# Optimization experiments

Measured on AMD Instinct MI355X. Metric: run time of the kernel, lower is better.

## Reference

```python
import jax, jax.numpy as jnp
import numpy as np

B = 64        # graphs per batch
N = 2048      # nodes per graph
BN = B * N
BE = BN * 16  # edges (avg degree 16)
C1 = 64
C2 = 64
M = 16
K_EDGES = 4   # hardcoded k=4 in original forward


def setup_inputs() -> dict:
    key = jax.random.key(0)
    k1, k2, k3, k4, k5, k6 = jax.random.split(key, 6)
    x = jax.random.normal(k1, (BN, C1), dtype=jnp.float32)
    e_ = jax.random.randint(k2, (2, BE), 0, BN, dtype=jnp.int32)
    b_ = jnp.repeat(jnp.arange(B, dtype=jnp.int32), N)  # sorted batch index
    # Linear params (stored as (in, out); torch stores (out, in))
    W_assign = jax.random.normal(k3, (C1, M), dtype=jnp.float32) / np.sqrt(C1)
    b_assign = jax.random.normal(k4, (M,), dtype=jnp.float32) * 0.01
    W_embed = jax.random.normal(k5, (C1, C2 - 3), dtype=jnp.float32) / np.sqrt(C1)
    b_embed = jax.random.normal(k6, (C2 - 3,), dtype=jnp.float32) * 0.01
    return {"x": x, "e_": e_, "b_": b_, "W_assign": W_assign,
            "b_assign": b_assign, "W_embed": W_embed, "b_embed": b_embed}


def reference(x, e_, b_, W_assign, b_assign, W_embed, b_embed):
    BN_, _ = x.shape
    Bn = int(jnp.max(b_)) + 1
    Mm = W_assign.shape[1]

    p = x[:, :3]                                   # (BN, 3) positions
    f = x @ W_embed + b_embed                      # (BN, C2-3)
    S = jax.nn.softmax(x @ W_assign + b_assign, axis=-1)  # (BN, M)

    # Weighted scatter-reduce pooling: index_add over (batch*M + m)
    # == per-batch segment_sum of S[n,m] * feat[n,c]
    Zf = jax.ops.segment_sum(S[:, :, None] * f[:, None, :], b_, num_segments=Bn)  # (B, M, C2-3)
    Zp = jax.ops.segment_sum(S[:, :, None] * p[:, None, :], b_, num_segments=Bn)  # (B, M, 3)
    w = jax.ops.segment_sum(S, b_, num_segments=Bn)                               # (B, M)
    w = jnp.maximum(w, 1e-10)
    Zp = Zp / w[..., None]
    x_out = jnp.concatenate([Zp, Zf], axis=-1).reshape(Bn * Mm, -1)  # (B*M, C2)

    # Sparse adjacency pooling: AS = A_NN @ S (A_NN[src,dst]=1 per edge)
    AS = jax.ops.segment_sum(S[e_[1]], e_[0], num_segments=BN_)  # (BN, M)
    # A_MM[b] = (S^T masked to batch b) @ AS
    A_MM = jax.ops.segment_sum(S[:, :, None] * AS[:, None, :], b_, num_segments=Bn)  # (B, M, M)

    # top-k edge construction on pooled adjacency
    dst = jax.lax.top_k(A_MM, K_EDGES)[1]                                # (B, M, k)
    src = jnp.broadcast_to(jnp.arange(Mm)[None, :, None], (Bn, Mm, K_EDGES))
    offset = (jnp.arange(Bn) * Mm)[:, None, None]
    e_out = jnp.stack([(src + offset).reshape(-1), (dst + offset).reshape(-1)], axis=0)
    b_out = jnp.repeat(jnp.arange(Bn), Mm)
    return x_out, e_out, b_out
```

## Files before the change

kernel.cpp:

```cpp
#include <hip/hip_runtime.h>

#define BN 131072
#define BE 2097152
#define NGR 64
#define CAP 36864

#define XS_OFF     0
#define WACC_OFF   262144
#define A_OFF      266240
#define ZERO_U4    20736
#define CUR_OFF    331776
#define QS_OFF     332032
#define ENDS_OFF   333056
#define SH_OFF     2430208
#define PK_OFF     6624512

__device__ __forceinline__ float bflo(unsigned u) { return __uint_as_float(u << 16); }
__device__ __forceinline__ float bfhi(unsigned u) { return __uint_as_float(u & 0xFFFF0000u); }

__global__ __launch_bounds__(256) void k_zero(uint4* __restrict__ zbase,
                                              int* __restrict__ cur)
{
    int zi = blockIdx.x * 256 + threadIdx.x;
    if (zi < ZERO_U4) zbase[zi] = make_uint4(0u, 0u, 0u, 0u);
    if (blockIdx.x == 0 && threadIdx.x < NGR) cur[threadIdx.x] = threadIdx.x * CAP;
}

__global__ __launch_bounds__(256) void k_scatter(const int* __restrict__ e_,
                                                 int* __restrict__ cur,
                                                 unsigned* __restrict__ packed)
{
    __shared__ int h[64];
    __shared__ int gb[64];
    int t = threadIdx.x;
    if (t < 64) h[t] = 0;
    __syncthreads();
    size_t base = (size_t)blockIdx.x * 4096;
    int e0v[16], e1v[16], rk[16];
    #pragma unroll
    for (int k = 0; k < 16; ++k) {
        size_t i = base + k * 256 + t;
        e0v[k] = e_[i];
        e1v[k] = e_[BE + i];
        rk[k] = atomicAdd(&h[e0v[k] >> 11], 1);
    }
    __syncthreads();
    if (t < 64) gb[t] = atomicAdd(&cur[t], h[t]);
    __syncthreads();
    #pragma unroll
    for (int k = 0; k < 16; ++k) {
        int b = e0v[k] >> 11;
        packed[gb[b] + rk[k]] = ((unsigned)(e0v[k] & 2047) << 17) | (unsigned)e1v[k];
    }
}

__global__ __launch_bounds__(256) void k_nodeSort(const float* __restrict__ x,
                                                  const float* __restrict__ Wa,
                                                  const float* __restrict__ ba,
                                                  unsigned short* __restrict__ Sh,
                                                  float* __restrict__ Xs,
                                                  float* __restrict__ wacc,
                                                  unsigned* __restrict__ packed,
                                                  const int* __restrict__ cur,
                                                  int* __restrict__ qs,
                                                  int* __restrict__ ends4)
{
    __shared__ __align__(16) unsigned char smem[47616];
    const int t = threadIdx.x;
    const int blk = blockIdx.x;

    if (blk < 256) {
        unsigned* sout = (unsigned*)smem;
        int* h    = (int*)(smem + 36864);
        int* psum = (int*)(smem + 45056);
        const int Q = blk;
        const int g = Q >> 2;
        const int q = Q & 3;
        const int slab = g * CAP;
        const int n = cur[g] - slab;
        const int chunk = (n + 3) >> 2;
        const int qlo = slab + min(q * chunk, n);
        const int qhi = slab + min((q + 1) * chunk, n);
        const int nq = qhi - qlo;
        if (t == 0) qs[Q] = qlo;

        for (int i = t; i < 2048; i += 256) h[i] = 0;
        __syncthreads();
        for (int i = t; i < nq; i += 256) {
            atomicAdd(&h[packed[qlo + i] >> 17], 1);
        }
        __syncthreads();

        int hl[8]; int s = 0;
        #pragma unroll
        for (int j = 0; j < 8; ++j) { hl[j] = h[t * 8 + j]; s += hl[j]; }
        psum[t] = s;
        __syncthreads();
        for (int off = 1; off < 256; off <<= 1) {
            int v = (t >= off) ? psum[t - off] : 0;
            __syncthreads();
            psum[t] += v;
            __syncthreads();
        }
        int run = psum[t] - s;
        int* ends = ends4 + (Q << 11);
        #pragma unroll
        for (int j = 0; j < 8; ++j) {
            int bin = t * 8 + j;
            int c = hl[j];
            h[bin] = run;
            run += c;
            ends[bin] = qlo + run;
        }
        __syncthreads();
        for (int i = t; i < nq; i += 256) {
            unsigned u = packed[qlo + i];
            int pos = atomicAdd(&h[u >> 17], 1);
            sout[pos] = u & 131071u;
        }
        __syncthreads();
        for (int i = t; i < nq; i += 256) packed[qlo + i] = sout[i];
        return;
    }

    const int nblk = blk - 256;
    const int g = nblk >> 4;
    float* Xl = (float*)smem;
    float* Sl = (float*)(smem + 33280);
    float* Wl = (float*)(smem + 43520);
    const int nd = t & 127;
    const int ch = t >> 7;

    const float4* xg4 = (const float4*)(x + (size_t)nblk * 128 * 64);
    #pragma unroll
    for (int it = 0; it < 8; ++it) {
        int idx4 = it * 256 + t;
        float4 v = xg4[idx4];
        int node = idx4 >> 4;
        int c4 = (idx4 & 15) * 4;
        float* p = &Xl[node * 65 + c4];
        p[0] = v.x; p[1] = v.y; p[2] = v.z; p[3] = v.w;
    }
    for (int i = t; i < 1024; i += 256) Wl[i] = Wa[i];
    __syncthreads();

    float lg[16];
    #pragma unroll
    for (int m = 0; m < 16; ++m) lg[m] = 0.f;
    const int c0 = ch * 32;
    for (int c = c0; c < c0 + 32; ++c) {
        float xc = Xl[nd * 65 + c];
        #pragma unroll
        for (int m = 0; m < 16; ++m) lg[m] += xc * Wl[c * 16 + m];
    }
    float* Pl = Sl;
    if (ch == 1) {
        #pragma unroll
        for (int m = 0; m < 16; ++m) Pl[nd * 17 + m] = lg[m];
    }
    __syncthreads();

    float s[16];
    if (ch == 0) {
        float sum = 0.f, mx;
        #pragma unroll
        for (int m = 0; m < 16; ++m) lg[m] += ba[m] + Pl[nd * 17 + m];
        mx = lg[0];
        #pragma unroll
        for (int m = 1; m < 16; ++m) mx = fmaxf(mx, lg[m]);
        #pragma unroll
        for (int m = 0; m < 16; ++m) { s[m] = __expf(lg[m] - mx); sum += s[m]; }
        float inv = 1.f / sum;
        #pragma unroll
        for (int m = 0; m < 16; ++m) s[m] *= inv;

        unsigned pk8[8];
        #pragma unroll
        for (int j = 0; j < 8; ++j) {
            unsigned b0 = __float_as_uint(s[2*j]);
            unsigned b1 = __float_as_uint(s[2*j+1]);
            unsigned h0 = (b0 + 0x7FFFu + ((b0 >> 16) & 1u)) >> 16;
            unsigned h1 = (b1 + 0x7FFFu + ((b1 >> 16) & 1u)) >> 16;
            pk8[j] = h0 | (h1 << 16);
        }
        uint4* hrow = (uint4*)(Sh + ((size_t)nblk * 128 + nd) * 16);
        hrow[0] = make_uint4(pk8[0], pk8[1], pk8[2], pk8[3]);
        hrow[1] = make_uint4(pk8[4], pk8[5], pk8[6], pk8[7]);
    }
    __syncthreads();
    if (ch == 0) {
        #pragma unroll
        for (int q = 0; q < 4; ++q)
            *(float4*)(&Sl[nd * 20 + q * 4]) = make_float4(s[q*4], s[q*4+1], s[q*4+2], s[q*4+3]);
    }
    __syncthreads();

    const int c = t & 63;
    const int mg = t >> 6;
    float a0 = 0.f, a1 = 0.f, a2 = 0.f, a3 = 0.f;
    for (int n = 0; n < 128; ++n) {
        float xv = Xl[n * 65 + c];
        float4 sa = *(const float4*)(&Sl[n * 20 + mg * 4]);
        a0 += sa.x * xv; a1 += sa.y * xv; a2 += sa.z * xv; a3 += sa.w * xv;
    }
    float* xsg = Xs + g * 1024 + (mg * 4) * 64 + c;
    atomicAdd(&xsg[0],   a0);
    atomicAdd(&xsg[64],  a1);
    atomicAdd(&xsg[128], a2);
    atomicAdd(&xsg[192], a3);

    if (t < 16) {
        float ws_ = 0.f;
        for (int n = 0; n < 128; ++n) ws_ += Sl[n * 20 + t];
        atomicAdd(&wacc[g * 16 + t], ws_);
    }
}

__global__ __launch_bounds__(256) void k_edge(const unsigned* __restrict__ se1,
                                              const unsigned short* __restrict__ Sh,
                                              const int* __restrict__ ends4,
                                              const int* __restrict__ qs,
                                              float* __restrict__ A)
{
    __shared__ __align__(16) float ASl[64 * 16];
    const int t = threadIdx.x;
    const int blk = blockIdx.x;
    const int g = blk >> 5;
    const int nbase = blk << 6;

    {
        const int qd = t >> 2;
        const int c4 = (t & 3) << 2;
        const int nl = (nbase & 2047) + qd;
        const unsigned short* __restrict__ ShB = Sh + c4;

        int lo[4], hi[4];
        #pragma unroll
        for (int q = 0; q < 4; ++q) {
            const int Qb = (g << 2) + q;
            const int* __restrict__ ends = ends4 + (Qb << 11);
            lo[q] = nl ? ends[nl - 1] : qs[Qb];
            hi[q] = ends[nl];
        }

        float a0 = 0.f, a1 = 0.f, a2 = 0.f, a3 = 0.f;
        #pragma unroll
        for (int q = 0; q < 4; ++q) {
            int i = lo[q];
            const int h2 = hi[q];
            for (; i + 4 <= h2; i += 4) {
                unsigned ea = se1[i];
                unsigned eb = se1[i + 1];
                unsigned ec = se1[i + 2];
                unsigned ed = se1[i + 3];
                uint2 ra = *(const uint2*)(ShB + ((size_t)ea << 4));
                uint2 rb = *(const uint2*)(ShB + ((size_t)eb << 4));
                uint2 rc = *(const uint2*)(ShB + ((size_t)ec << 4));
                uint2 rd = *(const uint2*)(ShB + ((size_t)ed << 4));
                a0 += bflo(ra.x) + bflo(rb.x) + bflo(rc.x) + bflo(rd.x);
                a1 += bfhi(ra.x) + bfhi(rb.x) + bfhi(rc.x) + bfhi(rd.x);
                a2 += bflo(ra.y) + bflo(rb.y) + bflo(rc.y) + bflo(rd.y);
                a3 += bfhi(ra.y) + bfhi(rb.y) + bfhi(rc.y) + bfhi(rd.y);
            }
            for (; i < h2; ++i) {
                unsigned ea = se1[i];
                uint2 ra = *(const uint2*)(ShB + ((size_t)ea << 4));
                a0 += bflo(ra.x); a1 += bfhi(ra.x); a2 += bflo(ra.y); a3 += bfhi(ra.y);
            }
        }
        *(float4*)(&ASl[qd * 16 + c4]) = make_float4(a0, a1, a2, a3);
    }
    __syncthreads();

    {
        const int m = t >> 4;
        const int k = t & 15;
        const unsigned short* __restrict__ SgM = Sh + ((size_t)nbase << 4) + m;
        float a = 0.f;
        #pragma unroll 4
        for (int i = 0; i < 64; ++i) {
            float sv = __uint_as_float((unsigned)SgM[(size_t)i << 4] << 16);
            a += sv * ASl[i * 16 + k];
        }
        atomicAdd(&A[(g << 8) + t], a);
    }
}

__global__ __launch_bounds__(256) void k_xt(const float* __restrict__ Xs,
                                            const float* __restrict__ wacc,
                                            const float* __restrict__ We,
                                            const float* __restrict__ be,
                                            const float* __restrict__ A,
                                            float* __restrict__ out)
{
    __shared__ float WeL[64 * 61];
    const int t = threadIdx.x;
    const int blk = blockIdx.x;
    for (int i = t; i < 64 * 61; i += 256) WeL[i] = We[i];
    __syncthreads();

    if (blk < 256) {
        int lane = t & 63;
        int row = blk * 4 + (t >> 6);
        const float* xs = Xs + row * 64;
        float w = wacc[row];
        float val;
        if (lane < 3) {
            val = xs[lane] / fmaxf(w, 1e-10f);
        } else {
            int c2 = lane - 3;
            float accv = w * be[c2];
            for (int cc = 0; cc < 64; ++cc) accv += xs[cc] * WeL[cc * 61 + c2];
            val = accv;
        }
        out[row * 64 + lane] = val;
    } else {
        int r = (blk - 256) * 256 + t;
        float v[16];
        #pragma unroll
        for (int i = 0; i < 16; ++i) v[i] = A[r * 16 + i];
        float* e0o = out + 65536;
        float* e1o = out + 65536 + 4096;
        float* bo  = out + 65536 + 8192;
        unsigned mask = 0;
        #pragma unroll
        for (int rep = 0; rep < 4; ++rep) {
            float best = -3.4e38f; int bi = 0;
            #pragma unroll
            for (int i = 0; i < 16; ++i) {
                bool ok = (((mask >> i) & 1u) == 0u) && (v[i] > best);
                if (ok) { best = v[i]; bi = i; }
            }
            mask |= (1u << bi);
            e0o[r * 4 + rep] = (float)r;
            e1o[r * 4 + rep] = (float)((r & ~15) + bi);
        }
        bo[r] = (float)(r >> 4);
    }
}

extern "C" void kernel_launch(void* const* d_in, const int* in_sizes, int n_in,
                              void* d_out, int out_size, void* d_ws, size_t ws_size,
                              hipStream_t stream)
{
    const float* x  = (const float*)d_in[0];
    const int*   e  = (const int*)d_in[1];
    const float* Wa = (const float*)d_in[3];
    const float* ba = (const float*)d_in[4];
    const float* We = (const float*)d_in[5];
    const float* be = (const float*)d_in[6];

    char* ws = (char*)d_ws;
    float* Xs     = (float*)(ws + XS_OFF);
    float* wacc   = (float*)(ws + WACC_OFF);
    float* A      = (float*)(ws + A_OFF);
    int*   cur    = (int*)(ws + CUR_OFF);
    int*   qs     = (int*)(ws + QS_OFF);
    int*   ends4  = (int*)(ws + ENDS_OFF);
    unsigned short* Sh = (unsigned short*)(ws + SH_OFF);
    unsigned* packed = (unsigned*)(ws + PK_OFF);

    k_zero    <<<82, 256, 0, stream>>>((uint4*)ws, cur);
    k_scatter <<<512, 256, 0, stream>>>(e, cur, packed);
    k_nodeSort<<<1280, 256, 0, stream>>>(x, Wa, ba, Sh, Xs, wacc, packed, cur, qs, ends4);
    k_edge    <<<2048, 256, 0, stream>>>(packed, Sh, ends4, qs, A);
    k_xt      <<<260, 256, 0, stream>>>(Xs, wacc, We, be, A, (float*)d_out);
}
```

Measured before the change: 87.87 us.

## Split edge sort into eighths and store node tile as bf16 in LDS

The per-graph edge sort now uses 8 sub-blocks per graph instead of 4, which halves the LDS sort buffer and doubles the number of sort blocks. The edge kernel now walks 8 segment ranges per node instead of 4. The node-softmax path keeps the x tile in LDS as packed bf16 rather than fp32, shrinking shared memory from about 47KB to 31KB so more blocks can be resident per CU. This lowers the precision of the logits and of the pooled features, and it adds more segment boundaries to read and more short loops in the edge kernel.

```diff
diff --git a/kernel.cpp b/kernel.cpp
--- a/kernel.cpp
+++ b/kernel.cpp
@@ -11,12 +11,19 @@
 #define ZERO_U4    20736
 #define CUR_OFF    331776
 #define QS_OFF     332032
-#define ENDS_OFF   333056
-#define SH_OFF     2430208
-#define PK_OFF     6624512
+#define ENDS_OFF   334080
+#define SH_OFF     4528384
+#define PK_OFF     8722688
 
 __device__ __forceinline__ float bflo(unsigned u) { return __uint_as_float(u << 16); }
 __device__ __forceinline__ float bfhi(unsigned u) { return __uint_as_float(u & 0xFFFF0000u); }
+__device__ __forceinline__ unsigned bfpack(float a, float b) {
+    unsigned b0 = __float_as_uint(a);
+    unsigned b1 = __float_as_uint(b);
+    unsigned h0 = (b0 + 0x7FFFu + ((b0 >> 16) & 1u)) >> 16;
+    unsigned h1 = (b1 + 0x7FFFu + ((b1 >> 16) & 1u)) >> 16;
+    return h0 | (h1 << 16);
+}
 
 __global__ __launch_bounds__(256) void k_zero(uint4* __restrict__ zbase,
                                               int* __restrict__ cur)
@@ -54,6 +61,7 @@
     }
 }
 
+#define SE_CAP 4864
 __global__ __launch_bounds__(256) void k_nodeSort(const float* __restrict__ x,
                                                   const float* __restrict__ Wa,
                                                   const float* __restrict__ ba,
@@ -63,22 +71,22 @@
                                                   unsigned* __restrict__ packed,
                                                   const int* __restrict__ cur,
                                                   int* __restrict__ qs,
-                                                  int* __restrict__ ends4)
-{
-    __shared__ __align__(16) unsigned char smem[47616];
+                                                  int* __restrict__ ends8)
+{
+    __shared__ __align__(16) unsigned char smem[31232];
     const int t = threadIdx.x;
     const int blk = blockIdx.x;
 
-    if (blk < 256) {
+    if (blk < 512) {
         unsigned* sout = (unsigned*)smem;
-        int* h    = (int*)(smem + 36864);
-        int* psum = (int*)(smem + 45056);
+        int* h    = (int*)(smem + 19456);
+        int* psum = (int*)(smem + 27648);
         const int Q = blk;
-        const int g = Q >> 2;
-        const int q = Q & 3;
+        const int g = Q >> 3;
+        const int q = Q & 7;
         const int slab = g * CAP;
         const int n = cur[g] - slab;
-        const int chunk = (n + 3) >> 2;
+        const int chunk = (n + 7) >> 3;
         const int qlo = slab + min(q * chunk, n);
         const int qhi = slab + min((q + 1) * chunk, n);
         const int nq = qhi - qlo;
@@ -103,7 +111,7 @@
             __syncthreads();
         }
         int run = psum[t] - s;
-        int* ends = ends4 + (Q << 11);
+        int* ends = ends8 + (Q << 11);
         #pragma unroll
         for (int j = 0; j < 8; ++j) {
             int bin = t * 8 + j;
@@ -123,11 +131,12 @@
         return;
     }
 
-    const int nblk = blk - 256;
+    const int nblk = blk - 512;
     const int g = nblk >> 4;
-    float* Xl = (float*)smem;
-    float* Sl = (float*)(smem + 33280);
-    float* Wl = (float*)(smem + 43520);
+    unsigned short* Xh = (unsigned short*)smem;
+    unsigned* Xh32 = (unsigned*)smem;
+    float* Sl = (float*)(smem + 16896);
+    float* Wl = (float*)(smem + 27136);
     const int nd = t & 127;
     const int ch = t >> 7;
 
@@ -137,9 +146,9 @@
         int idx4 = it * 256 + t;
         float4 v = xg4[idx4];
         int node = idx4 >> 4;
-        int c4 = (idx4 & 15) * 4;
-        float* p = &Xl[node * 65 + c4];
-        p[0] = v.x; p[1] = v.y; p[2] = v.z; p[3] = v.w;
+        int cp = (idx4 & 15) * 2;
+        Xh32[node * 33 + cp]     = bfpack(v.x, v.y);
+        Xh32[node * 33 + cp + 1] = bfpack(v.z, v.w);
     }
     for (int i = t; i < 1024; i += 256) Wl[i] = Wa[i];
     __syncthreads();
@@ -147,11 +156,13 @@
     float lg[16];
     #pragma unroll
     for (int m = 0; m < 16; ++m) lg[m] = 0.f;
-    const int c0 = ch * 32;
-    for (int c = c0; c < c0 + 32; ++c) {
-        float xc = Xl[nd * 65 + c];
-        #pragma unroll
-        for (int m = 0; m < 16; ++m) lg[m] += xc * Wl[c * 16 + m];
+    const int p0 = ch * 16;
+    for (int p = p0; p < p0 + 16; ++p) {
+        unsigned xp = Xh32[nd * 33 + p];
+        float x0 = bflo(xp), x1 = bfhi(xp);
+        const float* w0 = &Wl[(2 * p) * 16];
+        #pragma unroll
+        for (int m = 0; m < 16; ++m) lg[m] += x0 * w0[m] + x1 * w0[16 + m];
     }
     float* Pl = Sl;
     if (ch == 1) {
@@ -176,13 +187,7 @@
 
         unsigned pk8[8];
         #pragma unroll
-        for (int j = 0; j < 8; ++j) {
-            unsigned b0 = __float_as_uint(s[2*j]);
-            unsigned b1 = __float_as_uint(s[2*j+1]);
-            unsigned h0 = (b0 + 0x7FFFu + ((b0 >> 16) & 1u)) >> 16;
-            unsigned h1 = (b1 + 0x7FFFu + ((b1 >> 16) & 1u)) >> 16;
-            pk8[j] = h0 | (h1 << 16);
-        }
+        for (int j = 0; j < 8; ++j) pk8[j] = bfpack(s[2*j], s[2*j+1]);
         uint4* hrow = (uint4*)(Sh + ((size_t)nblk * 128 + nd) * 16);
         hrow[0] = make_uint4(pk8[0], pk8[1], pk8[2], pk8[3]);
         hrow[1] = make_uint4(pk8[4], pk8[5], pk8[6], pk8[7]);
@@ -199,7 +204,7 @@
     const int mg = t >> 6;
     float a0 = 0.f, a1 = 0.f, a2 = 0.f, a3 = 0.f;
     for (int n = 0; n < 128; ++n) {
-        float xv = Xl[n * 65 + c];
+        float xv = __uint_as_float((unsigned)Xh[n * 66 + c] << 16);
         float4 sa = *(const float4*)(&Sl[n * 20 + mg * 4]);
         a0 += sa.x * xv; a1 += sa.y * xv; a2 += sa.z * xv; a3 += sa.w * xv;
     }
@@ -218,7 +223,7 @@
 
 __global__ __launch_bounds__(256) void k_edge(const unsigned* __restrict__ se1,
                                               const unsigned short* __restrict__ Sh,
-                                              const int* __restrict__ ends4,
+                                              const int* __restrict__ ends8,
                                               const int* __restrict__ qs,
                                               float* __restrict__ A)
 {
@@ -234,18 +239,18 @@
         const int nl = (nbase & 2047) + qd;
         const unsigned short* __restrict__ ShB = Sh + c4;
 
-        int lo[4], hi[4];
-        #pragma unroll
-        for (int q = 0; q < 4; ++q) {
-            const int Qb = (g << 2) + q;
-            const int* __restrict__ ends = ends4 + (Qb << 11);
+        int lo[8], hi[8];
+        #pragma unroll
+        for (int q = 0; q < 8; ++q) {
+            const int Qb = (g << 3) + q;
+            const int* __restrict__ ends = ends8 + (Qb << 11);
             lo[q] = nl ? ends[nl - 1] : qs[Qb];
             hi[q] = ends[nl];
         }
 
         float a0 = 0.f, a1 = 0.f, a2 = 0.f, a3 = 0.f;
         #pragma unroll
-        for (int q = 0; q < 4; ++q) {
+        for (int q = 0; q < 8; ++q) {
             int i = lo[q];
             const int h2 = hi[q];
             for (; i + 4 <= h2; i += 4) {
@@ -356,13 +361,13 @@
     float* A      = (float*)(ws + A_OFF);
     int*   cur    = (int*)(ws + CUR_OFF);
     int*   qs     = (int*)(ws + QS_OFF);
-    int*   ends4  = (int*)(ws + ENDS_OFF);
+    int*   ends8  = (int*)(ws + ENDS_OFF);
     unsigned short* Sh = (unsigned short*)(ws + SH_OFF);
     unsigned* packed = (unsigned*)(ws + PK_OFF);
 
     k_zero    <<<82, 256, 0, stream>>>((uint4*)ws, cur);
     k_scatter <<<512, 256, 0, stream>>>(e, cur, packed);
-    k_nodeSort<<<1280, 256, 0, stream>>>(x, Wa, ba, Sh, Xs, wacc, packed, cur, qs, ends4);
-    k_edge    <<<2048, 256, 0, stream>>>(packed, Sh, ends4, qs, A);
+    k_nodeSort<<<1536, 256, 0, stream>>>(x, Wa, ba, Sh, Xs, wacc, packed, cur, qs, ends8);
+    k_edge    <<<2048, 256, 0, stream>>>(packed, Sh, ends8, qs, A);
     k_xt      <<<260, 256, 0, stream>>>(Xs, wacc, We, be, A, (float*)d_out);
 }
```

New measurement: 94.27 us. +7.3%, slower.

## Fuse final projection and top-k into producer kernels via last-block counters

Applied to the files above, without the earlier changes.

Removes the separate k_xt launch. The last block to finish each graph, detected with per-graph atomic done-counters, now runs the embedding projection in k_nodeSort and the top-k edge selection in k_edge. This saves one kernel launch and its dependency gap. In exchange it adds threadfences and atomics to every block, and the tail work for each graph runs serially in one block, with We read from global memory instead of LDS.

```diff
diff --git a/kernel.cpp b/kernel.cpp
--- a/kernel.cpp
+++ b/kernel.cpp
@@ -8,15 +8,24 @@
 #define XS_OFF     0
 #define WACC_OFF   262144
 #define A_OFF      266240
-#define ZERO_U4    20736
-#define CUR_OFF    331776
-#define QS_OFF     332032
-#define ENDS_OFF   333056
-#define SH_OFF     2430208
-#define PK_OFF     6624512
+#define NDONE_OFF  331776
+#define EDONE_OFF  332032
+#define ZERO_U4    20768
+#define CUR_OFF    332288
+#define QS_OFF     332544
+#define ENDS_OFF   333568
+#define SH_OFF     2430720
+#define PK_OFF     6625024
 
 __device__ __forceinline__ float bflo(unsigned u) { return __uint_as_float(u << 16); }
 __device__ __forceinline__ float bfhi(unsigned u) { return __uint_as_float(u & 0xFFFF0000u); }
+__device__ __forceinline__ unsigned bfpack(float a, float b) {
+    unsigned b0 = __float_as_uint(a);
+    unsigned b1 = __float_as_uint(b);
+    unsigned h0 = (b0 + 0x7FFFu + ((b0 >> 16) & 1u)) >> 16;
+    unsigned h1 = (b1 + 0x7FFFu + ((b1 >> 16) & 1u)) >> 16;
+    return h0 | (h1 << 16);
+}
 
 __global__ __launch_bounds__(256) void k_zero(uint4* __restrict__ zbase,
                                               int* __restrict__ cur)
@@ -63,9 +72,14 @@
                                                   unsigned* __restrict__ packed,
                                                   const int* __restrict__ cur,
                                                   int* __restrict__ qs,
-                                                  int* __restrict__ ends4)
+                                                  int* __restrict__ ends4,
+                                                  int* __restrict__ ndone,
+                                                  const float* __restrict__ We,
+                                                  const float* __restrict__ be,
+                                                  float* __restrict__ out)
 {
     __shared__ __align__(16) unsigned char smem[47616];
+    __shared__ int isLast;
     const int t = threadIdx.x;
     const int blk = blockIdx.x;
 
@@ -176,13 +190,7 @@
 
         unsigned pk8[8];
         #pragma unroll
-        for (int j = 0; j < 8; ++j) {
-            unsigned b0 = __float_as_uint(s[2*j]);
-            unsigned b1 = __float_as_uint(s[2*j+1]);
-            unsigned h0 = (b0 + 0x7FFFu + ((b0 >> 16) & 1u)) >> 16;
-            unsigned h1 = (b1 + 0x7FFFu + ((b1 >> 16) & 1u)) >> 16;
-            pk8[j] = h0 | (h1 << 16);
-        }
+        for (int j = 0; j < 8; ++j) pk8[j] = bfpack(s[2*j], s[2*j+1]);
         uint4* hrow = (uint4*)(Sh + ((size_t)nblk * 128 + nd) * 16);
         hrow[0] = make_uint4(pk8[0], pk8[1], pk8[2], pk8[3]);
         hrow[1] = make_uint4(pk8[4], pk8[5], pk8[6], pk8[7]);
@@ -214,15 +222,48 @@
         for (int n = 0; n < 128; ++n) ws_ += Sl[n * 20 + t];
         atomicAdd(&wacc[g * 16 + t], ws_);
     }
+
+    __threadfence();
+    __syncthreads();
+    if (t == 0) isLast = (atomicAdd(&ndone[g], 1) == 15);
+    __syncthreads();
+    if (isLast) {
+        __threadfence();
+        float* XsL = (float*)smem;
+        for (int i = t; i < 1024; i += 256) XsL[i] = Xs[(g << 10) + i];
+        __syncthreads();
+        #pragma unroll
+        for (int j = 0; j < 4; ++j) {
+            int idx = j * 256 + t;
+            int rl = idx >> 6;
+            int lane = idx & 63;
+            int row = (g << 4) + rl;
+            float w = wacc[row];
+            const float* xs = &XsL[rl * 64];
+            float val;
+            if (lane < 3) {
+                val = xs[lane] / fmaxf(w, 1e-10f);
+            } else {
+                int c2 = lane - 3;
+                float accv = w * be[c2];
+                for (int cc = 0; cc < 64; ++cc) accv += xs[cc] * We[cc * 61 + c2];
+                val = accv;
+            }
+            out[row * 64 + lane] = val;
+        }
+    }
 }
 
 __global__ __launch_bounds__(256) void k_edge(const unsigned* __restrict__ se1,
                                               const unsigned short* __restrict__ Sh,
                                               const int* __restrict__ ends4,
                                               const int* __restrict__ qs,
-                                              float* __restrict__ A)
+                                              float* __restrict__ A,
+                                              int* __restrict__ edone,
+                                              float* __restrict__ out)
 {
     __shared__ __align__(16) float ASl[64 * 16];
+    __shared__ int isLastE;
     const int t = threadIdx.x;
     const int blk = blockIdx.x;
     const int g = blk >> 5;
@@ -284,58 +325,36 @@
         }
         atomicAdd(&A[(g << 8) + t], a);
     }
-}
-
-__global__ __launch_bounds__(256) void k_xt(const float* __restrict__ Xs,
-                                            const float* __restrict__ wacc,
-                                            const float* __restrict__ We,
-                                            const float* __restrict__ be,
-                                            const float* __restrict__ A,
-                                            float* __restrict__ out)
-{
-    __shared__ float WeL[64 * 61];
-    const int t = threadIdx.x;
-    const int blk = blockIdx.x;
-    for (int i = t; i < 64 * 61; i += 256) WeL[i] = We[i];
-    __syncthreads();
-
-    if (blk < 256) {
-        int lane = t & 63;
-        int row = blk * 4 + (t >> 6);
-        const float* xs = Xs + row * 64;
-        float w = wacc[row];
-        float val;
-        if (lane < 3) {
-            val = xs[lane] / fmaxf(w, 1e-10f);
-        } else {
-            int c2 = lane - 3;
-            float accv = w * be[c2];
-            for (int cc = 0; cc < 64; ++cc) accv += xs[cc] * WeL[cc * 61 + c2];
-            val = accv;
-        }
-        out[row * 64 + lane] = val;
-    } else {
-        int r = (blk - 256) * 256 + t;
-        float v[16];
-        #pragma unroll
-        for (int i = 0; i < 16; ++i) v[i] = A[r * 16 + i];
-        float* e0o = out + 65536;
-        float* e1o = out + 65536 + 4096;
-        float* bo  = out + 65536 + 8192;
-        unsigned mask = 0;
-        #pragma unroll
-        for (int rep = 0; rep < 4; ++rep) {
-            float best = -3.4e38f; int bi = 0;
+
+    __threadfence();
+    __syncthreads();
+    if (t == 0) isLastE = (atomicAdd(&edone[g], 1) == 31);
+    __syncthreads();
+    if (isLastE) {
+        __threadfence();
+        if (t < 16) {
+            int r = (g << 4) + t;
+            float v[16];
             #pragma unroll
-            for (int i = 0; i < 16; ++i) {
-                bool ok = (((mask >> i) & 1u) == 0u) && (v[i] > best);
-                if (ok) { best = v[i]; bi = i; }
+            for (int i = 0; i < 16; ++i) v[i] = A[r * 16 + i];
+            float* e0o = out + 65536;
+            float* e1o = out + 65536 + 4096;
+            float* bo  = out + 65536 + 8192;
+            unsigned mask = 0;
+            #pragma unroll
+            for (int rep = 0; rep < 4; ++rep) {
+                float best = -3.4e38f; int bi = 0;
+                #pragma unroll
+                for (int i = 0; i < 16; ++i) {
+                    bool ok = (((mask >> i) & 1u) == 0u) && (v[i] > best);
+                    if (ok) { best = v[i]; bi = i; }
+                }
+                mask |= (1u << bi);
+                e0o[r * 4 + rep] = (float)r;
+                e1o[r * 4 + rep] = (float)((r & ~15) + bi);
             }
-            mask |= (1u << bi);
-            e0o[r * 4 + rep] = (float)r;
-            e1o[r * 4 + rep] = (float)((r & ~15) + bi);
-        }
-        bo[r] = (float)(r >> 4);
+            bo[r] = (float)(r >> 4);
+        }
     }
 }
 
@@ -354,6 +373,8 @@
     float* Xs     = (float*)(ws + XS_OFF);
     float* wacc   = (float*)(ws + WACC_OFF);
     float* A      = (float*)(ws + A_OFF);
+    int*   ndone  = (int*)(ws + NDONE_OFF);
+    int*   edone  = (int*)(ws + EDONE_OFF);
     int*   cur    = (int*)(ws + CUR_OFF);
     int*   qs     = (int*)(ws + QS_OFF);
     int*   ends4  = (int*)(ws + ENDS_OFF);
@@ -362,7 +383,7 @@
 
     k_zero    <<<82, 256, 0, stream>>>((uint4*)ws, cur);
     k_scatter <<<512, 256, 0, stream>>>(e, cur, packed);
-    k_nodeSort<<<1280, 256, 0, stream>>>(x, Wa, ba, Sh, Xs, wacc, packed, cur, qs, ends4);
-    k_edge    <<<2048, 256, 0, stream>>>(packed, Sh, ends4, qs, A);
-    k_xt      <<<260, 256, 0, stream>>>(Xs, wacc, We, be, A, (float*)d_out);
-}
+    k_nodeSort<<<1280, 256, 0, stream>>>(x, Wa, ba, Sh, Xs, wacc, packed, cur, qs, ends4,
+                                         ndone, We, be, (float*)d_out);
+    k_edge    <<<2048, 256, 0, stream>>>(packed, Sh, ends4, qs, A, edone, (float*)d_out);
+}
```

Measured after the change: 318.3 us. 262% more time.
